# Performance work log

Hardware: AMD Instinct MI355X
Metric: run time of the kernel (lower is better)

The kernel has to match this reference:

```python
import jax, jax.numpy as jnp
import numpy as np

EPS = 1e-5        # LayerNorm eps (torch default)
BETA = 1.0e12     # Hopfield scaling -> near-hard nearest-pattern retrieval


def _ln(x, g, b):
    mu = jnp.mean(x, axis=-1, keepdims=True)
    var = jnp.var(x, axis=-1, keepdims=True)
    return (x - mu) * jax.lax.rsqrt(var + EPS) * g + b


def setup_inputs() -> dict:
    key = jax.random.key(0)
    ks = jax.random.split(key, 10)
    B, S, D_IN, Q, P, D_OUT, N_CLS = 32768, 16, 14, 256, 256, 28, 7

    def n(k, shape, scale=1.0):
        return jax.random.normal(k, shape, dtype=jnp.float32) * scale

    return {
        "x": n(ks[0], (B, S, D_IN)),                 # (batch, bands=16, 14)
        "lookup": n(ks[1], (1, Q, D_IN)),            # learned stored patterns
        "g_st": jnp.ones((D_IN,), jnp.float32),      # LN stored pattern
        "b_st": jnp.zeros((D_IN,), jnp.float32),
        "g_sp": jnp.ones((D_IN,), jnp.float32),      # LN state pattern
        "b_sp": jnp.zeros((D_IN,), jnp.float32),
        "g_pp": jnp.ones((D_IN,), jnp.float32),      # LN pattern projection
        "b_pp": jnp.zeros((D_IN,), jnp.float32),
        "Wv": n(ks[2], (P, D_IN), 1.0 / np.sqrt(D_IN)),   # value proj 14->256 (no bias)
        "Wo": n(ks[3], (D_OUT, P), 1.0 / np.sqrt(P)),     # out proj 256->28 (no bias)
        "Wm": n(ks[4], (N_CLS, D_OUT), 1.0 / np.sqrt(D_OUT)),  # Linear_m 28->7
        "bm": n(ks[5], (N_CLS,), 0.1),
        "Wb": n(ks[6], (1, S), 1.0 / np.sqrt(S)),          # Linear_b 16->1
        "bb": n(ks[7], (1,), 0.1),
    }


def reference(x, lookup, g_st, b_st, g_sp, b_sp, g_pp, b_pp,
              Wv, Wo, Wm, bm, Wb, bb):
    # --- HopfieldLayer (num_heads=1, static Q/K, projected V) ---
    q = _ln(x, g_sp, b_sp)                       # state pattern, (B,S,14)
    k = _ln(lookup[0], g_st, b_st)               # stored patterns, (Q,14)
    v = _ln(lookup[0], g_pp, b_pp) @ Wv.T        # (Q,256)
    logits = BETA * jnp.einsum('bsd,qd->bsq', q, k)   # (B,S,Q)
    attn = jax.nn.softmax(logits, axis=-1)       # near one-hot retrieval
    h = jnp.einsum('bsq,qp->bsp', attn, v)       # (B,S,256)
    hop = h @ Wo.T                                # (B,S,28)
    # --- head ---
    y = hop @ Wm.T + bm                           # (B,S,7)
    y = jnp.swapaxes(y, 1, 2)                     # (B,7,S) == einsum 'abc->acb'
    z = y @ Wb.T + bb                             # (B,7,1)
    return jax.nn.softmax(z[:, :, 0], axis=1)     # (B,7)
```

## Files before the change

kernel.cpp:

```cpp
#include <hip/hip_runtime.h>
#include <math.h>

#define BATCH 32768
#define SS 16
#define DI 14
#define BQ 256
#define NC 7
#define NBLK 2048

#define BIAS 64.0f

#define WS_MPACK_OFF 0
#define WS_TF_OFF    28672
#define WS_ZB_OFF    35840
#define WS_CV_OFF    35896
#define WS_HC_OFF    37944
#define WS_BH_OFF    37952
#define WS_BL_OFF    46144
#define WS_END_TAB   54336

typedef float  f32x16 __attribute__((ext_vector_type(16)));
typedef short  s16x8  __attribute__((ext_vector_type(8)));
typedef float  v2f    __attribute__((ext_vector_type(2)));

__device__ __forceinline__ unsigned short bf16_rne(float f) {
    unsigned u = __float_as_uint(f);
    unsigned r = u + 0x7FFFu + ((u >> 16) & 1u);
    return (unsigned short)(r >> 16);
}
__device__ __forceinline__ float bf16_to_f32(unsigned short h) {
    return __uint_as_float(((unsigned)h) << 16);
}

__device__ __forceinline__ unsigned key32(float v, int j) {
    unsigned u = __float_as_uint(v);
    u ^= ((unsigned)((int)u >> 31)) | 0x80000000u;
    return (u & 0xFFFFFF00u) | (unsigned)(255 - j);
}

__global__ __launch_bounds__(256) void precompute_kernel(
    const float* __restrict__ lookup,
    const float* __restrict__ g_st, const float* __restrict__ b_st,
    const float* __restrict__ g_pp, const float* __restrict__ b_pp,
    const float* __restrict__ g_sp, const float* __restrict__ b_sp,
    const float* __restrict__ Wv,  const float* __restrict__ Wo,
    const float* __restrict__ Wm,  const float* __restrict__ bm,
    const float* __restrict__ Wb,  const float* __restrict__ bb,
    double2* __restrict__ mpack, float* __restrict__ Tf, double* __restrict__ zb,
    double* __restrict__ cvec, int* __restrict__ hc,
    s16x8* __restrict__ bfragH, s16x8* __restrict__ bfragL)
{
    __shared__ double G1s[256][7];
    __shared__ double Gs[14][7];
    const int tid = threadIdx.x;

    {
        const int p = tid;
        for (int c = 0; c < NC; ++c) {
            double acc = 0.0;
            for (int o = 0; o < 28; ++o)
                acc += (double)Wo[o * 256 + p] * (double)Wm[c * 28 + o];
            G1s[p][c] = acc;
        }
    }
    __syncthreads();
    if (tid < DI * NC) {
        const int d = tid / NC, c = tid % NC;
        double acc = 0.0;
        for (int p = 0; p < 256; ++p)
            acc += (double)Wv[p * DI + d] * G1s[p][c];
        Gs[d][c] = acc;
    }
    __syncthreads();

    {
        const int j = tid;
        double xr[DI];
        double sum = 0.0;
        for (int d = 0; d < DI; ++d) { xr[d] = (double)lookup[j * DI + d]; sum += xr[d]; }
        const double mu = sum * (1.0 / (double)DI);
        double vs = 0.0;
        for (int d = 0; d < DI; ++d) { const double t = xr[d] - mu; vs += t * t; }
        const double rs = 1.0 / sqrt(vs * (1.0 / (double)DI) + 1e-5);

        double kj[DI], vl[DI];
        for (int d = 0; d < DI; ++d) {
            const double nrm = (xr[d] - mu) * rs;
            kj[d] = nrm * (double)g_st[d] + (double)b_st[d];
            vl[d] = nrm * (double)g_pp[d] + (double)b_pp[d];
        }
        double mv[DI], S = 0.0, cj = 0.0;
        for (int d = 0; d < DI; ++d) {
            mv[d] = kj[d] * (double)g_sp[d];
            S += mv[d];
            cj += (double)b_sp[d] * kj[d];
        }
        const double Sm = S * (1.0 / (double)DI);
        for (int d2 = 0; d2 < DI / 2; ++d2) {
            double2 p; p.x = mv[2 * d2] - Sm; p.y = mv[2 * d2 + 1] - Sm;
            mpack[d2 * 256 + j] = p;
        }
        cvec[j] = cj;

        if (bfragH) {
            float mf[16];
            for (int d = 0; d < DI; ++d) mf[d] = (float)(mv[d] - Sm);
            mf[14] = (float)cj;
            mf[15] = BIAS;
            for (int ks = 0; ks < 2; ++ks) {
                s16x8 h8, l8;
                for (int i = 0; i < 8; ++i) {
                    const float f = mf[8 * ks + i];
                    const unsigned short h = bf16_rne(f);
                    const float r = f - bf16_to_f32(h);
                    h8[i] = (short)h;
                    l8[i] = (short)bf16_rne(r);
                }
                bfragH[(j >> 5) * 64 + ks * 32 + (j & 31)] = h8;
                bfragL[(j >> 5) * 64 + ks * 32 + (j & 31)] = l8;
            }
        }

        for (int c = 0; c < NC; ++c) {
            double acc = 0.0;
            for (int d = 0; d < DI; ++d) acc += vl[d] * Gs[d][c];
            Tf[j * NC + c] = (float)acc;
        }
    }
    if (tid < NC) {
        double wbsum = 0.0;
        for (int s = 0; s < SS; ++s) wbsum += (double)Wb[s];
        zb[tid] = (double)bm[tid] * wbsum + (double)bb[0];
    }
    if (tid == 0) {
        int f = 0;
        for (int d = 0; d < DI; ++d) f |= (b_sp[d] != 0.0f) ? 1 : 0;
        *hc = f;
    }
}

__global__ __launch_bounds__(256, 2) void hopfield_kernel(
    const float* __restrict__ x,
    const double2* __restrict__ mpack, const double* __restrict__ cvec,
    const int* __restrict__ hcp,
    const float* __restrict__ Tf, const double* __restrict__ zb,
    const float* __restrict__ Wb,
    const s16x8* __restrict__ bfH, const s16x8* __restrict__ bfL,
    const int use_tab,
    float* __restrict__ out)
{
    __shared__ s16x8  bhiS[8 * 64];
    __shared__ s16x8  bloS[8 * 64];
    __shared__ double zbs[NC];
    __shared__ float  wbs[SS];
    __shared__ int    jcandS[4][4][SS][2];
    __shared__ int    jstarS[4][4][SS];
    __shared__ double zrowd[4][4][NC];
    __shared__ float  irsS[4][4][SS];

    const int tid  = threadIdx.x;
    const int lane = tid & 63;
    const int w    = tid >> 6;
    const int hc   = *hcp;

    const int col  = lane & 31;
    const int khf  = lane >> 5;
    const int jadd = khf << 2;
    const int band = col & 15;
    const int biA  = col >> 4;

    const int gw = blockIdx.x * 4 + w;
    const float* xw = x + (size_t)gw * 4 * SS * DI;

    float xp[2][8];
    #pragma unroll
    for (int pr = 0; pr < 2; ++pr) {
        const int bi = pr * 2 + biA;
        const float* xr = xw + (bi * SS + band) * DI;
        if (khf == 0) {
            #pragma unroll
            for (int i = 0; i < 4; ++i) {
                const v2f p = *(const v2f*)(xr + 2 * i);
                xp[pr][2 * i] = p.x; xp[pr][2 * i + 1] = p.y;
            }
        } else {
            #pragma unroll
            for (int i = 0; i < 3; ++i) {
                const v2f p = *(const v2f*)(xr + 8 + 2 * i);
                xp[pr][2 * i] = p.x; xp[pr][2 * i + 1] = p.y;
            }
            xp[pr][6] = 0.f;
            xp[pr][7] = 1.0f;
        }
    }

    if (use_tab) {
        #pragma unroll
        for (int i = 0; i < 2; ++i) {
            const int idx = i * 256 + tid;
            bhiS[idx] = bfH[idx];
            bloS[idx] = bfL[idx];
        }
    } else {
        const int j = tid;
        float mf[16];
        #pragma unroll
        for (int d2 = 0; d2 < 7; ++d2) {
            const double2 mv = mpack[d2 * 256 + j];
            mf[2 * d2] = (float)mv.x; mf[2 * d2 + 1] = (float)mv.y;
        }
        mf[14] = (float)cvec[j];
        mf[15] = BIAS;
        #pragma unroll
        for (int ks = 0; ks < 2; ++ks) {
            s16x8 h8, l8;
            #pragma unroll
            for (int i = 0; i < 8; ++i) {
                const float f = mf[8 * ks + i];
                const unsigned short h = bf16_rne(f);
                const float r = f - bf16_to_f32(h);
                h8[i] = (short)h;
                l8[i] = (short)bf16_rne(r);
            }
            bhiS[(j >> 5) * 64 + ks * 32 + (j & 31)] = h8;
            bloS[(j >> 5) * 64 + ks * 32 + (j & 31)] = l8;
        }
    }
    if (tid < NC) zbs[tid] = zb[tid];
    if (tid < SS) wbs[tid] = Wb[tid];
    __syncthreads();

    if (hc) {
        const int bi = lane >> 4, s = lane & 15;
        const float* xr = xw + (bi * SS + s) * DI;
        float xv[DI]; float sum = 0.f;
        #pragma unroll
        for (int d = 0; d < DI; ++d) { xv[d] = xr[d]; sum += xv[d]; }
        const float mu = sum * (1.0f / (float)DI);
        float vs = 0.f;
        #pragma unroll
        for (int d = 0; d < DI; ++d) { const float t = xv[d] - mu; vs += t * t; }
        irsS[w][bi][s] = 1.0f / sqrtf(vs * (1.0f / (float)DI) + 1e-5f);
        __builtin_amdgcn_wave_barrier();
        if (khf == 1) {
            xp[0][6] = irsS[w][biA][band];
            xp[1][6] = irsS[w][2 + biA][band];
        }
    }

    #pragma unroll
    for (int pr = 0; pr < 2; ++pr) {
        const int bi = pr * 2 + biA;

        s16x8 xbh, xbl;
        #pragma unroll
        for (int i = 0; i < 8; ++i) {
            const float f = xp[pr][i];
            const unsigned short h = bf16_rne(f);
            const float r = f - bf16_to_f32(h);
            xbh[i] = (short)h;
            xbl[i] = (short)bf16_rne(r);
        }

        unsigned tv[16];
        #pragma unroll
        for (int r = 0; r < 16; ++r) tv[r] = 0u;

        f32x16 z16;
        #pragma unroll
        for (int r = 0; r < 16; ++r) z16[r] = 0.f;

        #pragma unroll
        for (int t = 0; t < 8; ++t) {
            const s16x8 ph = bhiS[t * 64 + lane];
            const s16x8 pl = bloS[t * 64 + lane];
            f32x16 acc = __builtin_amdgcn_mfma_f32_32x32x16_bf16(pl, xbh, z16, 0, 0, 0);
            acc = __builtin_amdgcn_mfma_f32_32x32x16_bf16(ph, xbl, acc, 0, 0, 0);
            acc = __builtin_amdgcn_mfma_f32_32x32x16_bf16(ph, xbh, acc, 0, 0, 0);
            #pragma unroll
            for (int r = 0; r < 16; ++r) {
                const unsigned tag = (__float_as_uint(acc[r]) & 0xFFFFFFF8u) | (unsigned)t;
                tv[r] = tv[r] > tag ? tv[r] : tag;
            }
        }

        unsigned hk[8], lk[8];
        #pragma unroll
        for (int r2 = 0; r2 < 8; ++r2) {
            const int ra = 2 * r2, rb = 2 * r2 + 1;
            const int ta = (int)(tv[ra] & 7u), tb = (int)(tv[rb] & 7u);
            const float fa = __uint_as_float(tv[ra] & 0xFFFFFFF8u) - BIAS;
            const float fb = __uint_as_float(tv[rb] & 0xFFFFFFF8u) - BIAS;
            const int ja = ta * 32 + ((ra & 3) + 8 * (ra >> 2)) + jadd;
            const int jb = tb * 32 + ((rb & 3) + 8 * (rb >> 2)) + jadd;
            const unsigned ka = key32(fa, ja);
            const unsigned kb = key32(fb, jb);
            hk[r2] = ka > kb ? ka : kb;
            lk[r2] = ka > kb ? kb : ka;
        }
        #pragma unroll
        for (int st = 4; st > 0; st >>= 1) {
            #pragma unroll
            for (int m = 0; m < 4; ++m) {
                if (m < st) {
                    const unsigned h1 = hk[m], h2 = hk[m + st];
                    const unsigned l1 = lk[m], l2 = lk[m + st];
                    const unsigned mn = h1 < h2 ? h1 : h2;
                    hk[m] = h1 > h2 ? h1 : h2;
                    const unsigned mx = l1 > l2 ? l1 : l2;
                    lk[m] = mn > mx ? mn : mx;
                }
            }
        }
        unsigned kh = hk[0], kl = lk[0];
        {
            const unsigned oh = (unsigned)__shfl_xor((int)kh, 32);
            const unsigned ol = (unsigned)__shfl_xor((int)kl, 32);
            const unsigned mn = kh < oh ? kh : oh;
            kh = kh > oh ? kh : oh;
            const unsigned mx = kl > ol ? kl : ol;
            kl = mn > mx ? mn : mx;
        }
        if (lane < 32) {
            jcandS[w][bi][band][0] = 255 - (int)(kh & 0xFFu);
            jcandS[w][bi][band][1] = 255 - (int)(kl & 0xFFu);
        }
    }
    __builtin_amdgcn_wave_barrier();

    #pragma unroll
    for (int u = 0; u < 2; ++u) {
        const int task = u * 64 + lane;
        const int bi = task >> 5, row = (task >> 1) & 15, ci = task & 1;
        const int j = jcandS[w][bi][row][ci];
        const float* xr = xw + (bi * SS + row) * DI;
        double a = 0.0;
        #pragma unroll
        for (int d2 = 0; d2 < 7; ++d2) {
            const v2f xpp = *(const v2f*)(xr + 2 * d2);
            const double2 mv = mpack[d2 * 256 + j];
            a += (double)xpp.x * mv.x + (double)xpp.y * mv.y;
        }
        if (hc) {
            double xv[DI]; double sum = 0.0;
            #pragma unroll
            for (int d = 0; d < DI; ++d) { xv[d] = (double)xr[d]; sum += xv[d]; }
            const double mu = sum * (1.0 / (double)DI);
            double vs = 0.0;
            #pragma unroll
            for (int d = 0; d < DI; ++d) { const double t = xv[d] - mu; vs += t * t; }
            const double irs64 = 1.0 / sqrt(vs * (1.0 / (double)DI) + 1e-5);
            a += irs64 * cvec[j];
        }
        const double oa = __shfl_xor(a, 1);
        const int    oj = __shfl_xor(j, 1);
        const int jwin = (a > oa || (a == oa && j < oj)) ? j : oj;
        if ((lane & 1) == 0) jstarS[w][bi][row] = jwin;
    }
    __builtin_amdgcn_wave_barrier();

    if (lane < 4 * NC) {
        const int bi = lane / NC, c = lane % NC;
        double zv = zbs[c];
        #pragma unroll
        for (int s = 0; s < SS; ++s)
            zv += (double)wbs[s] * (double)Tf[jstarS[w][bi][s] * NC + c];
        zrowd[w][bi][c] = zv;
    }
    __builtin_amdgcn_wave_barrier();
    if (lane < 4 * NC) {
        const int bi = lane / NC;
        double m = zrowd[w][bi][0];
        #pragma unroll
        for (int c2 = 1; c2 < NC; ++c2) m = fmax(m, zrowd[w][bi][c2]);
        float den = 0.f;
        #pragma unroll
        for (int c2 = 0; c2 < NC; ++c2) den += __expf((float)(zrowd[w][bi][c2] - m));
        const float num = __expf((float)(zrowd[w][bi][lane % NC] - m));
        out[(size_t)gw * 28 + lane] = num / den;
    }
}

extern "C" void kernel_launch(void* const* d_in, const int* in_sizes, int n_in,
                              void* d_out, int out_size, void* d_ws, size_t ws_size,
                              hipStream_t stream) {
    const float* x      = (const float*)d_in[0];
    const float* lookup = (const float*)d_in[1];
    const float* g_st   = (const float*)d_in[2];
    const float* b_st   = (const float*)d_in[3];
    const float* g_sp   = (const float*)d_in[4];
    const float* b_sp   = (const float*)d_in[5];
    const float* g_pp   = (const float*)d_in[6];
    const float* b_pp   = (const float*)d_in[7];
    const float* Wv     = (const float*)d_in[8];
    const float* Wo     = (const float*)d_in[9];
    const float* Wm     = (const float*)d_in[10];
    const float* bm     = (const float*)d_in[11];
    const float* Wb     = (const float*)d_in[12];
    const float* bb     = (const float*)d_in[13];

    double2* mpack = (double2*)((char*)d_ws + WS_MPACK_OFF);
    float*   Tf    = (float*)((char*)d_ws + WS_TF_OFF);
    double*  zbp   = (double*)((char*)d_ws + WS_ZB_OFF);
    double*  cvec  = (double*)((char*)d_ws + WS_CV_OFF);
    int*     hc    = (int*)((char*)d_ws + WS_HC_OFF);

    const int use_tab = (ws_size >= (size_t)WS_END_TAB) ? 1 : 0;
    s16x8* bfH = use_tab ? (s16x8*)((char*)d_ws + WS_BH_OFF) : (s16x8*)nullptr;
    s16x8* bfL = use_tab ? (s16x8*)((char*)d_ws + WS_BL_OFF) : (s16x8*)nullptr;

    precompute_kernel<<<1, 256, 0, stream>>>(lookup, g_st, b_st, g_pp, b_pp,
                                             g_sp, b_sp,
                                             Wv, Wo, Wm, bm, Wb, bb,
                                             mpack, Tf, zbp, cvec, hc, bfH, bfL);
    hopfield_kernel<<<NBLK, 256, 0, stream>>>(x, mpack, cvec, hc, Tf, zbp, Wb,
                                              bfH, bfL, use_tab,
                                              (float*)d_out);
}
```

Measured before the change: 133.6 us.

## Hold stored-pattern bf16 fragments in registers and drop block barrier

Each wave now loads its stored-pattern hi/lo bf16 MFMA fragments straight from global memory, or builds them, into registers instead of staging them through shared memory. This removes the __syncthreads, the shared tables and the per-tile LDS reads in the MFMA loop. zb and Wb are read directly from global. Launch bounds rise to 3 blocks per SM to raise occupancy. The trade-off is 64 extra VGPRs per lane, which could cause spills under the tighter register budget, and each wave now fetches the table redundantly from global/L2.

After: 207.6 us. +55.4%, slower.

```diff
diff --git a/kernel.cpp b/kernel.cpp
--- a/kernel.cpp
+++ b/kernel.cpp
@@ -139,7 +139,7 @@
     }
 }
 
-__global__ __launch_bounds__(256, 2) void hopfield_kernel(
+__global__ __launch_bounds__(256, 3) void hopfield_kernel(
     const float* __restrict__ x,
     const double2* __restrict__ mpack, const double* __restrict__ cvec,
     const int* __restrict__ hcp,
@@ -149,10 +149,6 @@
     const int use_tab,
     float* __restrict__ out)
 {
-    __shared__ s16x8  bhiS[8 * 64];
-    __shared__ s16x8  bloS[8 * 64];
-    __shared__ double zbs[NC];
-    __shared__ float  wbs[SS];
     __shared__ int    jcandS[4][4][SS][2];
     __shared__ int    jstarS[4][4][SS];
     __shared__ double zrowd[4][4][NC];
@@ -194,41 +190,42 @@
         }
     }
 
+    s16x8 fh[8], fl[8];
     if (use_tab) {
         #pragma unroll
-        for (int i = 0; i < 2; ++i) {
-            const int idx = i * 256 + tid;
-            bhiS[idx] = bfH[idx];
-            bloS[idx] = bfL[idx];
+        for (int t = 0; t < 8; ++t) {
+            fh[t] = bfH[t * 64 + lane];
+            fl[t] = bfL[t * 64 + lane];
         }
     } else {
-        const int j = tid;
-        float mf[16];
-        #pragma unroll
-        for (int d2 = 0; d2 < 7; ++d2) {
-            const double2 mv = mpack[d2 * 256 + j];
-            mf[2 * d2] = (float)mv.x; mf[2 * d2 + 1] = (float)mv.y;
-        }
-        mf[14] = (float)cvec[j];
-        mf[15] = BIAS;
-        #pragma unroll
-        for (int ks = 0; ks < 2; ++ks) {
-            s16x8 h8, l8;
+        #pragma unroll
+        for (int t = 0; t < 8; ++t) {
+            const int j = t * 32 + col;
+            float mf[8];
+            if (khf == 0) {
+                #pragma unroll
+                for (int d2 = 0; d2 < 4; ++d2) {
+                    const double2 mv = mpack[d2 * 256 + j];
+                    mf[2 * d2] = (float)mv.x; mf[2 * d2 + 1] = (float)mv.y;
+                }
+            } else {
+                #pragma unroll
+                for (int d2 = 0; d2 < 3; ++d2) {
+                    const double2 mv = mpack[(4 + d2) * 256 + j];
+                    mf[2 * d2] = (float)mv.x; mf[2 * d2 + 1] = (float)mv.y;
+                }
+                mf[6] = (float)cvec[j];
+                mf[7] = BIAS;
+            }
             #pragma unroll
             for (int i = 0; i < 8; ++i) {
-                const float f = mf[8 * ks + i];
-                const unsigned short h = bf16_rne(f);
-                const float r = f - bf16_to_f32(h);
-                h8[i] = (short)h;
-                l8[i] = (short)bf16_rne(r);
-            }
-            bhiS[(j >> 5) * 64 + ks * 32 + (j & 31)] = h8;
-            bloS[(j >> 5) * 64 + ks * 32 + (j & 31)] = l8;
-        }
-    }
-    if (tid < NC) zbs[tid] = zb[tid];
-    if (tid < SS) wbs[tid] = Wb[tid];
-    __syncthreads();
+                const unsigned short h = bf16_rne(mf[i]);
+                const float r = mf[i] - bf16_to_f32(h);
+                fh[t][i] = (short)h;
+                fl[t][i] = (short)bf16_rne(r);
+            }
+        }
+    }
 
     if (hc) {
         const int bi = lane >> 4, s = lane & 15;
@@ -272,11 +269,9 @@
 
         #pragma unroll
         for (int t = 0; t < 8; ++t) {
-            const s16x8 ph = bhiS[t * 64 + lane];
-            const s16x8 pl = bloS[t * 64 + lane];
-            f32x16 acc = __builtin_amdgcn_mfma_f32_32x32x16_bf16(pl, xbh, z16, 0, 0, 0);
-            acc = __builtin_amdgcn_mfma_f32_32x32x16_bf16(ph, xbl, acc, 0, 0, 0);
-            acc = __builtin_amdgcn_mfma_f32_32x32x16_bf16(ph, xbh, acc, 0, 0, 0);
+            f32x16 acc = __builtin_amdgcn_mfma_f32_32x32x16_bf16(fl[t], xbh, z16, 0, 0, 0);
+            acc = __builtin_amdgcn_mfma_f32_32x32x16_bf16(fh[t], xbl, acc, 0, 0, 0);
+            acc = __builtin_amdgcn_mfma_f32_32x32x16_bf16(fh[t], xbh, acc, 0, 0, 0);
             #pragma unroll
             for (int r = 0; r < 16; ++r) {
                 const unsigned tag = (__float_as_uint(acc[r]) & 0xFFFFFFF8u) | (unsigned)t;
@@ -361,10 +356,10 @@
 
     if (lane < 4 * NC) {
         const int bi = lane / NC, c = lane % NC;
-        double zv = zbs[c];
+        double zv = zb[c];
         #pragma unroll
         for (int s = 0; s < SS; ++s)
-            zv += (double)wbs[s] * (double)Tf[jstarS[w][bi][s] * NC + c];
+            zv += (double)Wb[s] * (double)Tf[jstarS[w][bi][s] * NC + c];
         zrowd[w][bi][c] = zv;
     }
     __builtin_amdgcn_wave_barrier();
```
